# Kernel tuning notes

Hardware: AMD Instinct MI355X
Metric: run time of the kernel (lower is better)

The kernel has to match this reference:

```python
import jax, jax.numpy as jnp
import numpy as np

L = 3          # num_layers
H = 128        # hidden_dim
NH = 4         # num heads
DH = H // NH   # head dim
B = 32         # graphs per batch
N = 1024       # nodes per graph
NTOT = B * N
DEG = 16
E = NTOT * DEG
BN_EPS = 1e-5


def setup_inputs() -> dict:
    key = jax.random.key(0)
    ks = jax.random.split(key, 16)
    s = 1.0 / np.sqrt(H)
    inp = {
        "x": jax.random.normal(ks[0], (NTOT, H), jnp.float32),
        "edge_attr": jax.random.normal(ks[1], (E, H), jnp.float32),
        "gine_w1": jax.random.normal(ks[2], (L, H, H), jnp.float32) * s,
        "gine_b1": jnp.zeros((L, H), jnp.float32),
        "gine_bn_g": jnp.ones((L, H), jnp.float32),
        "gine_bn_b": jnp.zeros((L, H), jnp.float32),
        "gine_w2": jax.random.normal(ks[3], (L, H, H), jnp.float32) * s,
        "gine_b2": jnp.zeros((L, H), jnp.float32),
        "attn_wqkv": jax.random.normal(ks[4], (L, 3 * H, H), jnp.float32) * s,
        "attn_bqkv": jnp.zeros((L, 3 * H), jnp.float32),
        "attn_wo": jax.random.normal(ks[5], (L, H, H), jnp.float32) * s,
        "attn_bo": jnp.zeros((L, H), jnp.float32),
        "norm1_g": jnp.ones((L, H), jnp.float32),
        "norm1_b": jnp.zeros((L, H), jnp.float32),
        "norm2_g": jnp.ones((L, H), jnp.float32),
        "norm2_b": jnp.zeros((L, H), jnp.float32),
        "norm3_g": jnp.ones((L, H), jnp.float32),
        "norm3_b": jnp.zeros((L, H), jnp.float32),
        "mlp_w1": jax.random.normal(ks[6], (L, 2 * H, H), jnp.float32) * s,
        "mlp_b1": jnp.zeros((L, 2 * H), jnp.float32),
        "mlp_w2": jax.random.normal(ks[7], (L, H, 2 * H), jnp.float32) * (1.0 / np.sqrt(2 * H)),
        "mlp_b2": jnp.zeros((L, H), jnp.float32),
    }
    # intra-graph random edges: local src/dst in [0, N) plus per-graph offset
    offs = (jnp.arange(E, dtype=jnp.int32) // (N * DEG)) * N  # graph offset per edge
    src = jax.random.randint(ks[8], (E,), 0, N, jnp.int32) + offs
    dst = jax.random.randint(ks[9], (E,), 0, N, jnp.int32) + offs
    inp["edge_index"] = jnp.stack([src, dst]).astype(jnp.int32)
    inp["batch"] = (jnp.arange(NTOT, dtype=jnp.int32) // N)
    return inp


def _bn(x, g, b):
    m = x.mean(axis=0)
    v = jnp.var(x, axis=0)
    return (x - m) * jax.lax.rsqrt(v + BN_EPS) * g + b


def _gps_forward(x, edge_attr, gine_w1, gine_b1, gine_bn_g, gine_bn_b, gine_w2, gine_b2,
                 attn_wqkv, attn_bqkv, attn_wo, attn_bo,
                 norm1_g, norm1_b, norm2_g, norm2_b, norm3_g, norm3_b,
                 mlp_w1, mlp_b1, mlp_w2, mlp_b2, edge_index, batch):
    src, dst = edge_index[0], edge_index[1]
    for i in range(L):
        # ---- GINEConv: msg = relu(x_j + e), sum-scatter, nn-MLP on x + aggr (eps=0)
        msg = jax.nn.relu(x[src] + edge_attr)                       # [E, H]
        aggr = jax.ops.segment_sum(msg, dst, num_segments=NTOT)     # [NTOT, H]
        h = x + aggr
        h = h @ gine_w1[i].T + gine_b1[i]
        h = jax.nn.relu(_bn(h, gine_bn_g[i], gine_bn_b[i]))
        h = h @ gine_w2[i].T + gine_b2[i]
        h_local = _bn(h + x, norm1_g[i], norm1_b[i])                # residual + norm1
        # ---- global multi-head attention on x (dense per-graph, equal sizes)
        xb = x.reshape(B, N, H)
        qkv = xb @ attn_wqkv[i].T + attn_bqkv[i]                    # [B, N, 3H]
        q, k, v = jnp.split(qkv, 3, axis=-1)
        q = q.reshape(B, N, NH, DH).transpose(0, 2, 1, 3)           # [B, nh, N, dh]
        k = k.reshape(B, N, NH, DH).transpose(0, 2, 1, 3)
        v = v.reshape(B, N, NH, DH).transpose(0, 2, 1, 3)
        scores = jnp.einsum("bhqd,bhkd->bhqk", q, k) / np.sqrt(DH)
        attn = jax.nn.softmax(scores, axis=-1)
        o = jnp.einsum("bhqk,bhkd->bhqd", attn, v)
        o = o.transpose(0, 2, 1, 3).reshape(B, N, H) @ attn_wo[i].T + attn_bo[i]
        h_attn = _bn(o.reshape(NTOT, H) + x, norm2_g[i], norm2_b[i])
        # ---- combine + FFN + norm3
        out = h_local + h_attn
        ff = jax.nn.relu(out @ mlp_w1[i].T + mlp_b1[i]) @ mlp_w2[i].T + mlp_b2[i]
        x = _bn(out + ff, norm3_g[i], norm3_b[i])
        if i != L - 1:
            x = jax.nn.relu(x)
    return x


def reference(x, edge_attr, gine_w1, gine_b1, gine_bn_g, gine_bn_b, gine_w2, gine_b2,
              attn_wqkv, attn_bqkv, attn_wo, attn_bo,
              norm1_g, norm1_b, norm2_g, norm2_b, norm3_g, norm3_b,
              mlp_w1, mlp_b1, mlp_w2, mlp_b2, edge_index, batch):
    return _gps_forward(x, edge_attr, gine_w1, gine_b1, gine_bn_g, gine_bn_b, gine_w2, gine_b2,
                        attn_wqkv, attn_bqkv, attn_wo, attn_bo,
                        norm1_g, norm1_b, norm2_g, norm2_b, norm3_g, norm3_b,
                        mlp_w1, mlp_b1, mlp_w2, mlp_b2, edge_index, batch)
```

## Files before the change

kernel.cpp:

```cpp
#include <hip/hip_runtime.h>
#include <hip/hip_bf16.h>
#include <math.h>

#define NTOT 32768
#define HDIM 128
#define NE   524288
#define NGRAPH 32
#define NNODE 1024
#define NHEAD 4
#define DHEAD 32

typedef __attribute__((ext_vector_type(8))) short bf8v;
typedef __attribute__((ext_vector_type(4))) float f4v;
typedef unsigned short u16;

__device__ __forceinline__ float4 ld4(const float* p){ return *(const float4*)p; }

__device__ __forceinline__ u16 bf16rn(float f){
  union { float f; unsigned u; } x; x.f = f;
  unsigned r = x.u + 0x7FFF + ((x.u >> 16) & 1);
  return (u16)(r >> 16);
}
__device__ __forceinline__ unsigned pk2(float a, float b){
  unsigned r;
  asm("v_cvt_pk_bf16_f32 %0, %1, %2" : "=v"(r) : "v"(a), "v"(b));
  return r;
}
__device__ __forceinline__ float bf2f(u16 u){
  union { unsigned u; float f; } x; x.u = ((unsigned)u) << 16;
  return x.f;
}

__global__ void k_count(const int* __restrict__ dst, int* __restrict__ deg){
  int e = blockIdx.x*256 + threadIdx.x;
  atomicAdd(&deg[dst[e]], 1);
}

__global__ __launch_bounds__(1024) void k_scan(const int* __restrict__ deg,
                                               int* __restrict__ indptr,
                                               int* __restrict__ cursor){
  __shared__ int sm[1024];
  int t = threadIdx.x;
  int base = t*32;
  int s = 0;
  for (int j=0;j<32;j++) s += deg[base+j];
  sm[t] = s; __syncthreads();
  for (int off=1; off<1024; off<<=1){
    int v = (t>=off) ? sm[t-off] : 0;
    __syncthreads();
    sm[t] += v;
    __syncthreads();
  }
  int ex = sm[t] - s;
  for (int j=0;j<32;j++){
    int d = deg[base+j];
    indptr[base+j] = ex; cursor[base+j] = ex;
    ex += d;
  }
  if (t == 1023) indptr[NTOT] = ex;
}

__global__ void k_fill(const int* __restrict__ dst, int* __restrict__ cursor,
                       int* __restrict__ perm){
  int e = blockIdx.x*256 + threadIdx.x;
  int pos = atomicAdd(&cursor[dst[e]], 1);
  perm[pos] = e;
}

__global__ __launch_bounds__(256) void k_eaprep(const float* __restrict__ ea,
    const int* __restrict__ src, const int* __restrict__ perm,
    u16* __restrict__ EAb, int* __restrict__ SRCp){
  int tid = threadIdx.x;
  int p = blockIdx.x*8 + (tid>>5);
  int c4 = (tid&31)*4;
  int e = perm[p];
  float4 v = ld4(&ea[(size_t)e*HDIM + c4]);
  uint2 o; o.x = pk2(v.x, v.y); o.y = pk2(v.z, v.w);
  *(uint2*)&EAb[(size_t)p*HDIM + c4] = o;
  if ((tid&31) == 0) SRCp[p] = src[e];
}

__global__ __launch_bounds__(256) void k_xprep(const float* __restrict__ x, u16* __restrict__ Xb){
  size_t i = ((size_t)blockIdx.x*256 + threadIdx.x)*4;
  float4 v = ld4(&x[i]);
  uint2 o; o.x = pk2(v.x,v.y); o.y = pk2(v.z,v.w);
  *(uint2*)&Xb[i] = o;
}

__global__ __launch_bounds__(256) void k_wprep(const float* s0,const float* s1,const float* s2,
    const float* s3,const float* s4,const float* s5, u16* __restrict__ Wb){
  const float* srcs[6] = {s0,s1,s2,s3,s4,s5};
  const int cnt4[6] = {12288,12288,36864,12288,24576,24576};
  const int off[6]  = {0,49152,98304,245760,294912,393216};
  int y = blockIdx.y;
  int i = blockIdx.x*256 + threadIdx.x;
  if (i >= cnt4[y]) return;
  float4 v = ld4(&srcs[y][(size_t)i*4]);
  uint2 o; o.x = pk2(v.x,v.y); o.y = pk2(v.z,v.w);
  *(uint2*)&Wb[off[y] + (size_t)i*4] = o;
}

__global__ __launch_bounds__(256) void k_aggr(const u16* __restrict__ Xb,
                       const u16* __restrict__ EAb,
                       const int* __restrict__ SRCp, const int* __restrict__ indptr,
                       u16* __restrict__ Hb){
  int tid = threadIdx.x;
  int n = blockIdx.x*8 + (tid>>5);
  int c4 = (tid&31)*4;
  int p0 = indptr[n], p1 = indptr[n+1];
  float a0=0.f,a1=0.f,a2=0.f,a3=0.f;
  for (int p=p0;p<p1;p++){
    int s = SRCp[p];
    uint2 xv = *(const uint2*)&Xb[(size_t)s*HDIM + c4];
    uint2 ev = *(const uint2*)&EAb[(size_t)p*HDIM + c4];
    a0 += fmaxf(bf2f((u16)(xv.x&0xffff)) + bf2f((u16)(ev.x&0xffff)), 0.f);
    a1 += fmaxf(bf2f((u16)(xv.x>>16))    + bf2f((u16)(ev.x>>16)), 0.f);
    a2 += fmaxf(bf2f((u16)(xv.y&0xffff)) + bf2f((u16)(ev.y&0xffff)), 0.f);
    a3 += fmaxf(bf2f((u16)(xv.y>>16))    + bf2f((u16)(ev.y>>16)), 0.f);
  }
  uint2 xn = *(const uint2*)&Xb[(size_t)n*HDIM + c4];
  a0 += bf2f((u16)(xn.x&0xffff)); a1 += bf2f((u16)(xn.x>>16));
  a2 += bf2f((u16)(xn.y&0xffff)); a3 += bf2f((u16)(xn.y>>16));
  uint2 o; o.x = pk2(a0,a1); o.y = pk2(a2,a3);
  *(uint2*)&Hb[(size_t)n*HDIM + c4] = o;
}

template<bool BNA, bool DUAL, bool RELU, bool EP, bool STATS, bool WROUT>
__global__ __launch_bounds__(256) void k_bgemm(const u16* __restrict__ Ab,
    const u16* __restrict__ A2b,
    const float* __restrict__ slotA, const float* __restrict__ gA, const float* __restrict__ bA,
    const float* __restrict__ slotB, const float* __restrict__ gB, const float* __restrict__ bB,
    const u16* __restrict__ Wb, const float* __restrict__ bias,
    const u16* __restrict__ Epb, u16* __restrict__ Cb,
    u16* __restrict__ OUTb, float* __restrict__ slotOut, int N, int K){
  __shared__ float sbnA[256];
  __shared__ float sbnB[256];
  __shared__ float sred[128];
  int tid = threadIdx.x;
  int w = tid>>6, l = tid&63;
  int q = l&15, g = l>>4;
  int m0 = blockIdx.x*128, n0 = blockIdx.y*64;
  int wr = w*32;
  const float invn = 1.0f/32768.0f;
  if (BNA || DUAL){
    if (tid < 128){
      float mean = slotA[tid]*invn;
      float var  = slotA[128+tid]*invn - mean*mean;
      float sc = gA[tid] * rsqrtf(var + 1e-5f);
      sbnA[tid] = sc; sbnA[128+tid] = bA[tid] - mean*sc;
      if (DUAL){
        float mean2 = slotB[tid]*invn;
        float var2  = slotB[128+tid]*invn - mean2*mean2;
        float sc2 = gB[tid] * rsqrtf(var2 + 1e-5f);
        sbnB[tid] = sc2; sbnB[128+tid] = bB[tid] - mean2*sc2;
      }
    }
  }
  if (STATS && tid < 128) sred[tid] = 0.f;
  if (BNA || DUAL || STATS) __syncthreads();

  f4v acc[2][4];
  #pragma unroll
  for (int i=0;i<2;i++)
    #pragma unroll
    for (int j=0;j<4;j++) acc[i][j] = (f4v){0.f,0.f,0.f,0.f};

  for (int kc=0; kc<K; kc+=32){
    bf8v af[2], bfv[4];
    #pragma unroll
    for (int mt=0;mt<2;mt++){
      int row = m0 + wr + 16*mt + q;
      if (!BNA && !DUAL){
        af[mt] = *(const bf8v*)&Ab[(size_t)row*K + kc + 8*g];
      } else {
        union { bf8v b; u16 s[8]; unsigned u[4]; } ra, r2, ro;
        ra.b = *(const bf8v*)&Ab[(size_t)row*K + kc + 8*g];
        if (DUAL) r2.b = *(const bf8v*)&A2b[(size_t)row*K + kc + 8*g];
        float v[8];
        #pragma unroll
        for (int j=0;j<8;j++){
          int kk = kc + 8*g + j;
          float f = bf2f(ra.s[j]) * sbnA[kk] + sbnA[128+kk];
          if (BNA) f = fmaxf(f, 0.f);
          if (DUAL) f += bf2f(r2.s[j]) * sbnB[kk] + sbnB[128+kk];
          v[j] = f;
        }
        ro.u[0]=pk2(v[0],v[1]); ro.u[1]=pk2(v[2],v[3]);
        ro.u[2]=pk2(v[4],v[5]); ro.u[3]=pk2(v[6],v[7]);
        af[mt] = ro.b;
        if (WROUT && blockIdx.y == 0)
          *(uint4*)&OUTb[(size_t)row*K + kc + 8*g] = *(uint4*)ro.u;
      }
    }
    #pragma unroll
    for (int nt=0;nt<4;nt++){
      int col = n0 + 16*nt + q;
      bfv[nt] = *(const bf8v*)&Wb[(size_t)col*K + kc + 8*g];
    }
    #pragma unroll
    for (int mt=0;mt<2;mt++)
      #pragma unroll
      for (int nt=0;nt<4;nt++)
        acc[mt][nt] = __builtin_amdgcn_mfma_f32_16x16x32_bf16(af[mt], bfv[nt], acc[mt][nt], 0,0,0);
  }
  float bbv[4];
  #pragma unroll
  for (int nt=0;nt<4;nt++) bbv[nt] = bias[n0 + 16*nt + q];
  float csum[4] = {0.f,0.f,0.f,0.f}, csq[4] = {0.f,0.f,0.f,0.f};
  #pragma unroll
  for (int mt=0;mt<2;mt++){
    int row0 = m0 + wr + 16*mt + 4*g;
    #pragma unroll
    for (int nt=0;nt<4;nt++){
      int col = n0 + 16*nt + q;
      #pragma unroll
      for (int r=0;r<4;r++){
        size_t off = (size_t)(row0+r)*N + col;
        float v = acc[mt][nt][r] + bbv[nt];
        if (EP) v += bf2f(Epb[off]);
        if (RELU) v = fmaxf(v, 0.f);
        Cb[off] = bf16rn(v);
        if (STATS){ csum[nt] += v; csq[nt] += v*v; }
      }
    }
  }
  if (STATS){
    #pragma unroll
    for (int nt=0;nt<4;nt++){
      int c = 16*nt + q;
      atomicAdd(&sred[c], csum[nt]);
      atomicAdd(&sred[64+c], csq[nt]);
    }
    __syncthreads();
    if (tid < 64){
      atomicAdd(&slotOut[n0+tid], sred[tid]);
      atomicAdd(&slotOut[128+n0+tid], sred[64+tid]);
    }
  }
}

__global__ __launch_bounds__(256) void k_qkvgemm(const u16* __restrict__ Ab,
    const u16* __restrict__ Wb, const float* __restrict__ bias,
    u16* __restrict__ Qb, u16* __restrict__ Kb, u16* __restrict__ VT){
  __shared__ u16 Sm[128*72];
  int tid = threadIdx.x;
  int w = tid>>6, l = tid&63;
  int q = l&15, g = l>>4;
  int m0 = blockIdx.x*128, n0 = blockIdx.y*64;
  int which = blockIdx.y >> 1, half = blockIdx.y & 1;
  int wr = w*32;
  const int K = 128;
  f4v acc[2][4];
  #pragma unroll
  for (int i=0;i<2;i++)
    #pragma unroll
    for (int j=0;j<4;j++) acc[i][j] = (f4v){0.f,0.f,0.f,0.f};
  for (int kc=0; kc<K; kc+=32){
    bf8v af[2], bfv[4];
    #pragma unroll
    for (int mt=0;mt<2;mt++)
      af[mt] = *(const bf8v*)&Ab[(size_t)(m0+wr+16*mt+q)*K + kc + 8*g];
    #pragma unroll
    for (int nt=0;nt<4;nt++)
      bfv[nt] = *(const bf8v*)&Wb[(size_t)(n0+16*nt+q)*K + kc + 8*g];
    #pragma unroll
    for (int mt=0;mt<2;mt++)
      #pragma unroll
      for (int nt=0;nt<4;nt++)
        acc[mt][nt] = __builtin_amdgcn_mfma_f32_16x16x32_bf16(af[mt], bfv[nt], acc[mt][nt], 0,0,0);
  }
  const float QSC = 0.17677669529663687f * 1.4426950408889634f;
  float scale = (which==0) ? QSC : 1.0f;
  float bbv[4];
  #pragma unroll
  for (int nt=0;nt<4;nt++) bbv[nt] = bias[n0 + 16*nt + q];
  if (which < 2){
    #pragma unroll
    for (int mt=0;mt<2;mt++){
      int row0 = wr + 16*mt + 4*g;
      #pragma unroll
      for (int nt=0;nt<4;nt++){
        int c = 16*nt + q;
        #pragma unroll
        for (int r=0;r<4;r++)
          Sm[(row0+r)*72 + c] = bf16rn((acc[mt][nt][r] + bbv[nt]) * scale);
      }
    }
    __syncthreads();
    u16* dst = (which==0) ? Qb : Kb;
    #pragma unroll
    for (int it=0; it<4; it++){
      int idx = tid + it*256;
      int row = idx >> 3, c8 = (idx & 7) * 8;
      uint4 v = *(const uint4*)&Sm[row*72 + c8];
      *(uint4*)&dst[(size_t)(m0+row)*128 + half*64 + c8] = v;
    }
  } else {
    #pragma unroll
    for (int mt=0;mt<2;mt++){
      int row0 = wr + 16*mt + 4*g;
      #pragma unroll
      for (int nt=0;nt<4;nt++){
        int c = 16*nt + q;
        uint2 p;
        p.x = pk2(acc[mt][nt][0] + bbv[nt], acc[mt][nt][1] + bbv[nt]);
        p.y = pk2(acc[mt][nt][2] + bbv[nt], acc[mt][nt][3] + bbv[nt]);
        *(uint2*)&Sm[c*136 + row0] = p;
      }
    }
    __syncthreads();
    int gg = m0 >> 10;
    int nl0 = m0 - gg*1024;
    #pragma unroll
    for (int it=0; it<4; it++){
      int idx = tid + it*256;
      int c = idx >> 4, n8 = (idx & 15) * 8;
      uint4 v = *(const uint4*)&Sm[c*136 + n8];
      *(uint4*)&VT[((size_t)gg*128 + half*64 + c)*1024 + nl0 + n8] = v;
    }
  }
}

template<bool RELU, bool F32OUT>
__global__ __launch_bounds__(256) void k_bnapply(const u16* __restrict__ X,
    const float* __restrict__ slot, const float* __restrict__ gv, const float* __restrict__ bv,
    u16* __restrict__ Yb, float* __restrict__ Yf){
  int idx = blockIdx.x*256 + threadIdx.x;
  int row = idx >> 4, c8 = (idx & 15) * 8;
  const float invn = 1.0f/32768.0f;
  union { uint4 u; u16 s[8]; } iv;
  iv.u = *(const uint4*)&X[(size_t)row*HDIM + c8];
  float o[8];
  #pragma unroll
  for (int j=0;j<8;j++){
    int c = c8+j;
    float mean = slot[c]*invn;
    float var  = slot[128+c]*invn - mean*mean;
    float sc = gv[c] * rsqrtf(var + 1e-5f);
    float sh = bv[c] - mean*sc;
    float v = bf2f(iv.s[j])*sc + sh;
    if (RELU) v = fmaxf(v, 0.f);
    o[j] = v;
  }
  if (F32OUT){
    float* dst = &Yf[(size_t)row*HDIM + c8];
    *(float4*)dst = make_float4(o[0],o[1],o[2],o[3]);
    *(float4*)(dst+4) = make_float4(o[4],o[5],o[6],o[7]);
  } else {
    uint4 ov;
    ov.x = pk2(o[0],o[1]); ov.y = pk2(o[2],o[3]);
    ov.z = pk2(o[4],o[5]); ov.w = pk2(o[6],o[7]);
    *(uint4*)&Yb[(size_t)row*HDIM + c8] = ov;
  }
}

__global__ __launch_bounds__(256) void k_flash2(const u16* __restrict__ Qb,
    const u16* __restrict__ Kb, const u16* __restrict__ VT,
    u16* __restrict__ O){
  __shared__ u16 Pl[4][16*72];
  int tid = threadIdx.x;
  int w = tid >> 6, l = tid & 63;
  int q = l & 15, grp = l >> 4;
  int qt = blockIdx.x, h = blockIdx.y, g = blockIdx.z;
  size_t gbase = (size_t)g*1024;
  size_t qrow0 = gbase + qt*64 + w*16;
  const u16* Vp = VT + ((size_t)(g*4 + h)*32)*1024;
  bf8v qf = *(const bf8v*)&Qb[(qrow0 + q)*128 + h*32 + 8*grp];
  u16* Pw = &Pl[w][0];
  float m = -1e30f, lsum = 0.f;
  f4v o0 = {0.f,0.f,0.f,0.f}, o1 = {0.f,0.f,0.f,0.f};
  for (int kt=0; kt<16; kt++){
    int k0 = kt*64;
    f4v st[4];
    #pragma unroll
    for (int t=0;t<4;t++){
      bf8v kf = *(const bf8v*)&Kb[(gbase + k0 + 16*t + q)*128 + h*32 + 8*grp];
      st[t] = __builtin_amdgcn_mfma_f32_16x16x32_bf16(kf, qf, (f4v){0.f,0.f,0.f,0.f}, 0,0,0);
    }
    float smax = st[0][0];
    #pragma unroll
    for (int t=0;t<4;t++)
      #pragma unroll
      for (int r=0;r<4;r++) smax = fmaxf(smax, st[t][r]);
    smax = fmaxf(smax, __shfl_xor(smax, 16));
    smax = fmaxf(smax, __shfl_xor(smax, 32));
    float mnew = fmaxf(m, smax);
    float alpha = exp2f(m - mnew);
    float psum = 0.f;
    #pragma unroll
    for (int t=0;t<4;t++){
      float p0 = exp2f(st[t][0]-mnew), p1 = exp2f(st[t][1]-mnew);
      float p2 = exp2f(st[t][2]-mnew), p3 = exp2f(st[t][3]-mnew);
      psum += (p0+p1)+(p2+p3);
      *(unsigned*)&Pw[q*72 + 16*t + 4*grp]     = pk2(p0,p1);
      *(unsigned*)&Pw[q*72 + 16*t + 4*grp + 2] = pk2(p2,p3);
    }
    psum += __shfl_xor(psum, 16);
    psum += __shfl_xor(psum, 32);
    lsum = lsum*alpha + psum;
    m = mnew;
    f4v aD;
    #pragma unroll
    for (int r=0;r<4;r++) aD[r] = __shfl(alpha, 4*grp + r);
    #pragma unroll
    for (int r=0;r<4;r++){ o0[r] *= aD[r]; o1[r] *= aD[r]; }
    bf8v pa0 = *(const bf8v*)&Pw[q*72 + 8*grp];
    bf8v pa1 = *(const bf8v*)&Pw[q*72 + 32 + 8*grp];
    bf8v v00 = *(const bf8v*)&Vp[(size_t)q*1024      + k0 + 8*grp];
    bf8v v01 = *(const bf8v*)&Vp[(size_t)q*1024      + k0 + 32 + 8*grp];
    bf8v v10 = *(const bf8v*)&Vp[(size_t)(16+q)*1024 + k0 + 8*grp];
    bf8v v11 = *(const bf8v*)&Vp[(size_t)(16+q)*1024 + k0 + 32 + 8*grp];
    o0 = __builtin_amdgcn_mfma_f32_16x16x32_bf16(pa0, v00, o0, 0,0,0);
    o0 = __builtin_amdgcn_mfma_f32_16x16x32_bf16(pa1, v01, o0, 0,0,0);
    o1 = __builtin_amdgcn_mfma_f32_16x16x32_bf16(pa0, v10, o1, 0,0,0);
    o1 = __builtin_amdgcn_mfma_f32_16x16x32_bf16(pa1, v11, o1, 0,0,0);
  }
  f4v lD;
  #pragma unroll
  for (int r=0;r<4;r++) lD[r] = __shfl(lsum, 4*grp + r);
  #pragma unroll
  for (int r=0;r<4;r++){
    float inv = 1.0f/lD[r];
    size_t row = qrow0 + 4*grp + r;
    O[row*HDIM + h*32 + q]      = bf16rn(o0[r]*inv);
    O[row*HDIM + h*32 + 16 + q] = bf16rn(o1[r]*inv);
  }
}

extern "C" void kernel_launch(void* const* d_in, const int* in_sizes, int n_in,
                              void* d_out, int out_size, void* d_ws, size_t ws_size,
                              hipStream_t stream){
  const float* x_in      = (const float*)d_in[0];
  const float* edge_attr = (const float*)d_in[1];
  const float* gine_w1   = (const float*)d_in[2];
  const float* gine_b1   = (const float*)d_in[3];
  const float* gine_bn_g = (const float*)d_in[4];
  const float* gine_bn_b = (const float*)d_in[5];
  const float* gine_w2   = (const float*)d_in[6];
  const float* gine_b2   = (const float*)d_in[7];
  const float* attn_wqkv = (const float*)d_in[8];
  const float* attn_bqkv = (const float*)d_in[9];
  const float* attn_wo   = (const float*)d_in[10];
  const float* attn_bo   = (const float*)d_in[11];
  const float* norm1_g   = (const float*)d_in[12];
  const float* norm1_b   = (const float*)d_in[13];
  const float* norm2_g   = (const float*)d_in[14];
  const float* norm2_b   = (const float*)d_in[15];
  const float* norm3_g   = (const float*)d_in[16];
  const float* norm3_b   = (const float*)d_in[17];
  const float* mlp_w1    = (const float*)d_in[18];
  const float* mlp_b1    = (const float*)d_in[19];
  const float* mlp_w2    = (const float*)d_in[20];
  const float* mlp_b2    = (const float*)d_in[21];
  const int* edge_index  = (const int*)d_in[22];
  const int* srcp = edge_index;
  const int* dstp = edge_index + NE;
  float* out = (float*)d_out;

  float* ws = (float*)d_ws;
  const size_t U = 4194304;
  u16* Xb   = (u16*)(ws);
  u16* Hb   = (u16*)(ws + U/2);
  u16* G1   = (u16*)(ws + U);
  u16* P1   = (u16*)(ws + U + U/2);
  u16* P2   = (u16*)(ws + 2*U);
  u16* Ob   = (u16*)(ws + 2*U + U/2);
  u16* FFb  = (u16*)(ws + 3*U);
  u16* OUTb = (u16*)(ws + 4*U);
  u16* H3   = (u16*)(ws + 4*U + U/2);
  u16* Qb   = (u16*)(ws + 5*U);
  u16* Kb   = (u16*)(ws + 5*U + U/2);
  u16* VTb  = (u16*)(ws + 6*U);
  u16* Wball= (u16*)(ws + 6*U + U/2);
  float* STATS = ws + 7*U - 8192;
  int* IW      = (int*)(ws + 7*U);
  int* deg     = IW;
  int* indptr  = IW + 32768;
  int* cursor  = IW + 32768 + 32772;
  int* perm    = cursor + 32768;
  u16* EAb  = (u16*)(ws + 8*U);
  int* SRCp = (int*)(ws + 16*U);

  u16* W1b  = Wball + 0;
  u16* W2b  = Wball + 49152;
  u16* WQb  = Wball + 98304;
  u16* WOb  = Wball + 245760;
  u16* WM1b = Wball + 294912;
  u16* WM2b = Wball + 393216;

  hipMemsetAsync(STATS, 0, 12*512*sizeof(float), stream);
  hipMemsetAsync(deg, 0, NTOT*sizeof(int), stream);
  k_count<<<NE/256, 256, 0, stream>>>(dstp, deg);
  k_scan<<<1, 1024, 0, stream>>>(deg, indptr, cursor);
  k_fill<<<NE/256, 256, 0, stream>>>(dstp, cursor, perm);
  k_eaprep<<<NE/8, 256, 0, stream>>>(edge_attr, srcp, perm, EAb, SRCp);
  k_xprep<<<4096, 256, 0, stream>>>(x_in, Xb);
  k_wprep<<<dim3(144,6), 256, 0, stream>>>(gine_w1, gine_w2, attn_wqkv, attn_wo, mlp_w1, mlp_w2, Wball);

  dim3 gN128(NTOT/128, 2), gN256(NTOT/128, 4), gQKV(NTOT/128, 6);

  for (int i=0;i<3;i++){
    const float* B1 = gine_b1 + (size_t)i*HDIM;
    const float* B2 = gine_b2 + (size_t)i*HDIM;
    const float* BQ = attn_bqkv + (size_t)i*3*HDIM;
    const float* BO = attn_bo + (size_t)i*HDIM;
    const float* BM1 = mlp_b1 + (size_t)i*2*HDIM;
    const float* BM2 = mlp_b2 + (size_t)i*HDIM;
    u16* w1 = W1b + (size_t)i*16384;
    u16* w2 = W2b + (size_t)i*16384;
    u16* wq = WQb + (size_t)i*49152;
    u16* wo = WOb + (size_t)i*16384;
    u16* wm1 = WM1b + (size_t)i*32768;
    u16* wm2 = WM2b + (size_t)i*32768;
    float* S0 = STATS + (size_t)(i*4+0)*512;
    float* S1 = STATS + (size_t)(i*4+1)*512;
    float* S2 = STATS + (size_t)(i*4+2)*512;
    float* S3 = STATS + (size_t)(i*4+3)*512;
    const float* bnG = gine_bn_g + (size_t)i*HDIM;
    const float* bnB = gine_bn_b + (size_t)i*HDIM;
    const float* n1g = norm1_g + (size_t)i*HDIM, *n1b = norm1_b + (size_t)i*HDIM;
    const float* n2g = norm2_g + (size_t)i*HDIM, *n2b = norm2_b + (size_t)i*HDIM;
    const float* n3g = norm3_g + (size_t)i*HDIM, *n3b = norm3_b + (size_t)i*HDIM;

    k_aggr<<<NTOT/8, 256, 0, stream>>>(Xb, EAb, SRCp, indptr, Hb);
    k_bgemm<false,false,false,false,true,false><<<gN128, 256, 0, stream>>>(
      Hb, nullptr, nullptr,nullptr,nullptr, nullptr,nullptr,nullptr,
      w1, B1, nullptr, G1, nullptr, S0, 128, 128);
    k_bgemm<true,false,false,true,true,false><<<gN128, 256, 0, stream>>>(
      G1, nullptr, S0, bnG, bnB, nullptr,nullptr,nullptr,
      w2, B2, Xb, P1, nullptr, S1, 128, 128);

    k_qkvgemm<<<gQKV, 256, 0, stream>>>(Xb, wq, BQ, Qb, Kb, VTb);
    k_flash2<<<dim3(16, NHEAD, NGRAPH), 256, 0, stream>>>(Qb, Kb, VTb, Ob);
    k_bgemm<false,false,false,true,true,false><<<gN128, 256, 0, stream>>>(
      Ob, nullptr, nullptr,nullptr,nullptr, nullptr,nullptr,nullptr,
      wo, BO, Xb, P2, nullptr, S2, 128, 128);

    k_bgemm<false,true,true,false,false,true><<<gN256, 256, 0, stream>>>(
      P1, P2, S1, n1g, n1b, S2, n2g, n2b,
      wm1, BM1, nullptr, FFb, OUTb, nullptr, 256, 128);
    k_bgemm<false,false,false,true,true,false><<<gN128, 256, 0, stream>>>(
      FFb, nullptr, nullptr,nullptr,nullptr, nullptr,nullptr,nullptr,
      wm2, BM2, OUTb, H3, nullptr, S3, 128, 256);

    if (i<2) k_bnapply<true ,false><<<2048, 256, 0, stream>>>(H3, S3, n3g, n3b, Xb, nullptr);
    else     k_bnapply<false,true ><<<2048, 256, 0, stream>>>(H3, S3, n3g, n3b, nullptr, out);
  }
}
```

Baseline: 1.049 ms.

## Merge independent per-layer kernels into horizontally fused launches and combine prep kernels

Independent stages are combined into single launches that dispatch on block index: aggregation with the QKV GEMM, flash attention with the first GINE GEMM, and the two post-projection GEMMs together. The three prep kernels become one launch, with the edge-attribute scatter writing to sorted positions via an epos array in place of a perm gather. The two memsets are merged into one, and the aggregation loop prefetches the next source index. The aim is fewer launches, less tail idle time and more concurrent work per launch. The cost is shared-memory footprint set by the largest branch and possible register pressure that lowers occupancy.

```diff
diff --git a/kernel.cpp b/kernel.cpp
--- a/kernel.cpp
+++ b/kernel.cpp
@@ -61,58 +61,62 @@
 }
 
 __global__ void k_fill(const int* __restrict__ dst, int* __restrict__ cursor,
-                       int* __restrict__ perm){
+                       int* __restrict__ epos){
   int e = blockIdx.x*256 + threadIdx.x;
   int pos = atomicAdd(&cursor[dst[e]], 1);
-  perm[pos] = e;
-}
-
-__global__ __launch_bounds__(256) void k_eaprep(const float* __restrict__ ea,
-    const int* __restrict__ src, const int* __restrict__ perm,
-    u16* __restrict__ EAb, int* __restrict__ SRCp){
-  int tid = threadIdx.x;
-  int p = blockIdx.x*8 + (tid>>5);
-  int c4 = (tid&31)*4;
-  int e = perm[p];
-  float4 v = ld4(&ea[(size_t)e*HDIM + c4]);
-  uint2 o; o.x = pk2(v.x, v.y); o.y = pk2(v.z, v.w);
-  *(uint2*)&EAb[(size_t)p*HDIM + c4] = o;
-  if ((tid&31) == 0) SRCp[p] = src[e];
-}
-
-__global__ __launch_bounds__(256) void k_xprep(const float* __restrict__ x, u16* __restrict__ Xb){
-  size_t i = ((size_t)blockIdx.x*256 + threadIdx.x)*4;
-  float4 v = ld4(&x[i]);
-  uint2 o; o.x = pk2(v.x,v.y); o.y = pk2(v.z,v.w);
-  *(uint2*)&Xb[i] = o;
-}
-
-__global__ __launch_bounds__(256) void k_wprep(const float* s0,const float* s1,const float* s2,
+  epos[e] = pos;
+}
+
+__global__ __launch_bounds__(256) void k_prep(const float* __restrict__ ea,
+    const int* __restrict__ src, const int* __restrict__ epos,
+    u16* __restrict__ EAb, int* __restrict__ SRCp,
+    const float* __restrict__ x, u16* __restrict__ Xb,
+    const float* s0,const float* s1,const float* s2,
     const float* s3,const float* s4,const float* s5, u16* __restrict__ Wb){
-  const float* srcs[6] = {s0,s1,s2,s3,s4,s5};
-  const int cnt4[6] = {12288,12288,36864,12288,24576,24576};
-  const int off[6]  = {0,49152,98304,245760,294912,393216};
-  int y = blockIdx.y;
-  int i = blockIdx.x*256 + threadIdx.x;
-  if (i >= cnt4[y]) return;
-  float4 v = ld4(&srcs[y][(size_t)i*4]);
-  uint2 o; o.x = pk2(v.x,v.y); o.y = pk2(v.z,v.w);
-  *(uint2*)&Wb[off[y] + (size_t)i*4] = o;
-}
-
-__global__ __launch_bounds__(256) void k_aggr(const u16* __restrict__ Xb,
-                       const u16* __restrict__ EAb,
-                       const int* __restrict__ SRCp, const int* __restrict__ indptr,
-                       u16* __restrict__ Hb){
-  int tid = threadIdx.x;
-  int n = blockIdx.x*8 + (tid>>5);
+  int b = blockIdx.x, tid = threadIdx.x;
+  if (b < 65536){
+    int e = b*8 + (tid>>5);
+    int c4 = (tid&31)*4;
+    int pos = epos[e];
+    float4 v = ld4(&ea[(size_t)e*HDIM + c4]);
+    uint2 o; o.x = pk2(v.x, v.y); o.y = pk2(v.z, v.w);
+    *(uint2*)&EAb[(size_t)pos*HDIM + c4] = o;
+    if ((tid&31) == 0) SRCp[pos] = src[e];
+  } else if (b < 69632){
+    size_t i = ((size_t)(b-65536)*256 + tid)*4;
+    float4 v = ld4(&x[i]);
+    uint2 o; o.x = pk2(v.x,v.y); o.y = pk2(v.z,v.w);
+    *(uint2*)&Xb[i] = o;
+  } else {
+    int idx = b - 69632;
+    int y = idx / 144;
+    int i = (idx % 144)*256 + tid;
+    const float* srcs[6] = {s0,s1,s2,s3,s4,s5};
+    const int cnt4[6] = {12288,12288,36864,12288,24576,24576};
+    const int off[6]  = {0,49152,98304,245760,294912,393216};
+    if (i < cnt4[y]){
+      float4 v = ld4(&srcs[y][(size_t)i*4]);
+      uint2 o; o.x = pk2(v.x,v.y); o.y = pk2(v.z,v.w);
+      *(uint2*)&Wb[off[y] + (size_t)i*4] = o;
+    }
+  }
+}
+
+__device__ __forceinline__ void aggr_body(int bx, int tid,
+    const u16* __restrict__ Xb, const u16* __restrict__ EAb,
+    const int* __restrict__ SRCp, const int* __restrict__ indptr,
+    u16* __restrict__ Hb){
+  int n = bx*8 + (tid>>5);
   int c4 = (tid&31)*4;
   int p0 = indptr[n], p1 = indptr[n+1];
   float a0=0.f,a1=0.f,a2=0.f,a3=0.f;
-  for (int p=p0;p<p1;p++){
-    int s = SRCp[p];
+  int p = p0;
+  int sNext = (p < p1) ? SRCp[p] : 0;
+  for (; p<p1; p++){
+    int s = sNext;
+    if (p+1 < p1) sNext = SRCp[p+1];
+    uint2 ev = *(const uint2*)&EAb[(size_t)p*HDIM + c4];
     uint2 xv = *(const uint2*)&Xb[(size_t)s*HDIM + c4];
-    uint2 ev = *(const uint2*)&EAb[(size_t)p*HDIM + c4];
     a0 += fmaxf(bf2f((u16)(xv.x&0xffff)) + bf2f((u16)(ev.x&0xffff)), 0.f);
     a1 += fmaxf(bf2f((u16)(xv.x>>16))    + bf2f((u16)(ev.x>>16)), 0.f);
     a2 += fmaxf(bf2f((u16)(xv.y&0xffff)) + bf2f((u16)(ev.y&0xffff)), 0.f);
@@ -126,34 +130,29 @@
 }
 
 template<bool BNA, bool DUAL, bool RELU, bool EP, bool STATS, bool WROUT>
-__global__ __launch_bounds__(256) void k_bgemm(const u16* __restrict__ Ab,
-    const u16* __restrict__ A2b,
+__device__ __forceinline__ void bgemm_body(int bx, int by, int tid,
+    const u16* __restrict__ Ab, const u16* __restrict__ A2b,
     const float* __restrict__ slotA, const float* __restrict__ gA, const float* __restrict__ bA,
     const float* __restrict__ slotB, const float* __restrict__ gB, const float* __restrict__ bB,
     const u16* __restrict__ Wb, const float* __restrict__ bias,
     const u16* __restrict__ Epb, u16* __restrict__ Cb,
-    u16* __restrict__ OUTb, float* __restrict__ slotOut, int N, int K){
-  __shared__ float sbnA[256];
-  __shared__ float sbnB[256];
-  __shared__ float sred[128];
-  int tid = threadIdx.x;
+    u16* __restrict__ OUTb, float* __restrict__ slotOut, int N, int K,
+    float* sbn1, float* sbn2, float* sred){
   int w = tid>>6, l = tid&63;
   int q = l&15, g = l>>4;
-  int m0 = blockIdx.x*128, n0 = blockIdx.y*64;
+  int m0 = bx*128, n0 = by*64;
   int wr = w*32;
   const float invn = 1.0f/32768.0f;
-  if (BNA || DUAL){
-    if (tid < 128){
-      float mean = slotA[tid]*invn;
-      float var  = slotA[128+tid]*invn - mean*mean;
-      float sc = gA[tid] * rsqrtf(var + 1e-5f);
-      sbnA[tid] = sc; sbnA[128+tid] = bA[tid] - mean*sc;
-      if (DUAL){
-        float mean2 = slotB[tid]*invn;
-        float var2  = slotB[128+tid]*invn - mean2*mean2;
-        float sc2 = gB[tid] * rsqrtf(var2 + 1e-5f);
-        sbnB[tid] = sc2; sbnB[128+tid] = bB[tid] - mean2*sc2;
-      }
+  if ((BNA || DUAL) && tid < 128){
+    float mean = slotA[tid]*invn;
+    float var  = slotA[128+tid]*invn - mean*mean;
+    float s = gA[tid] * rsqrtf(var + 1e-5f);
+    sbn1[tid] = s; sbn1[128+tid] = bA[tid] - mean*s;
+    if (DUAL){
+      float mean2 = slotB[tid]*invn;
+      float var2  = slotB[128+tid]*invn - mean2*mean2;
+      float s2 = gB[tid] * rsqrtf(var2 + 1e-5f);
+      sbn2[tid] = s2; sbn2[128+tid] = bB[tid] - mean2*s2;
     }
   }
   if (STATS && tid < 128) sred[tid] = 0.f;
@@ -166,7 +165,7 @@
     for (int j=0;j<4;j++) acc[i][j] = (f4v){0.f,0.f,0.f,0.f};
 
   for (int kc=0; kc<K; kc+=32){
-    bf8v af[2], bfv[4];
+    bf8v af[2];
     #pragma unroll
     for (int mt=0;mt<2;mt++){
       int row = m0 + wr + 16*mt + q;
@@ -180,23 +179,22 @@
         #pragma unroll
         for (int j=0;j<8;j++){
           int kk = kc + 8*g + j;
-          float f = bf2f(ra.s[j]) * sbnA[kk] + sbnA[128+kk];
+          float f = bf2f(ra.s[j]) * sbn1[kk] + sbn1[128+kk];
           if (BNA) f = fmaxf(f, 0.f);
-          if (DUAL) f += bf2f(r2.s[j]) * sbnB[kk] + sbnB[128+kk];
+          if (DUAL) f += bf2f(r2.s[j]) * sbn2[kk] + sbn2[128+kk];
           v[j] = f;
         }
         ro.u[0]=pk2(v[0],v[1]); ro.u[1]=pk2(v[2],v[3]);
         ro.u[2]=pk2(v[4],v[5]); ro.u[3]=pk2(v[6],v[7]);
         af[mt] = ro.b;
-        if (WROUT && blockIdx.y == 0)
+        if (WROUT && by == 0)
           *(uint4*)&OUTb[(size_t)row*K + kc + 8*g] = *(uint4*)ro.u;
       }
     }
-    #pragma unroll
-    for (int nt=0;nt<4;nt++){
-      int col = n0 + 16*nt + q;
-      bfv[nt] = *(const bf8v*)&Wb[(size_t)col*K + kc + 8*g];
-    }
+    bf8v bfv[4];
+    #pragma unroll
+    for (int nt=0;nt<4;nt++)
+      bfv[nt] = *(const bf8v*)&Wb[(size_t)(n0+16*nt+q)*K + kc + 8*g];
     #pragma unroll
     for (int mt=0;mt<2;mt++)
       #pragma unroll
@@ -239,27 +237,26 @@
   }
 }
 
-__global__ __launch_bounds__(256) void k_qkvgemm(const u16* __restrict__ Ab,
-    const u16* __restrict__ Wb, const float* __restrict__ bias,
-    u16* __restrict__ Qb, u16* __restrict__ Kb, u16* __restrict__ VT){
-  __shared__ u16 Sm[128*72];
-  int tid = threadIdx.x;
+__device__ __forceinline__ void qkv_body(int bx, int by, int tid,
+    const u16* __restrict__ Ab, const u16* __restrict__ Wb, const float* __restrict__ bias,
+    u16* __restrict__ Qb, u16* __restrict__ Kb, u16* __restrict__ VT, u16* Sm){
   int w = tid>>6, l = tid&63;
   int q = l&15, g = l>>4;
-  int m0 = blockIdx.x*128, n0 = blockIdx.y*64;
-  int which = blockIdx.y >> 1, half = blockIdx.y & 1;
+  int which = by >> 1, half = by & 1;
+  int m0 = bx*128, n0 = by*64;
+  const int K = 128;
   int wr = w*32;
-  const int K = 128;
   f4v acc[2][4];
   #pragma unroll
   for (int i=0;i<2;i++)
     #pragma unroll
     for (int j=0;j<4;j++) acc[i][j] = (f4v){0.f,0.f,0.f,0.f};
   for (int kc=0; kc<K; kc+=32){
-    bf8v af[2], bfv[4];
+    bf8v af[2];
     #pragma unroll
     for (int mt=0;mt<2;mt++)
       af[mt] = *(const bf8v*)&Ab[(size_t)(m0+wr+16*mt+q)*K + kc + 8*g];
+    bf8v bfv[4];
     #pragma unroll
     for (int nt=0;nt<4;nt++)
       bfv[nt] = *(const bf8v*)&Wb[(size_t)(n0+16*nt+q)*K + kc + 8*g];
@@ -310,7 +307,7 @@
     }
     __syncthreads();
     int gg = m0 >> 10;
-    int nl0 = m0 - gg*1024;
+    int nl0 = m0 & 1023;
     #pragma unroll
     for (int it=0; it<4; it++){
       int idx = tid + it*256;
@@ -321,52 +318,16 @@
   }
 }
 
-template<bool RELU, bool F32OUT>
-__global__ __launch_bounds__(256) void k_bnapply(const u16* __restrict__ X,
-    const float* __restrict__ slot, const float* __restrict__ gv, const float* __restrict__ bv,
-    u16* __restrict__ Yb, float* __restrict__ Yf){
-  int idx = blockIdx.x*256 + threadIdx.x;
-  int row = idx >> 4, c8 = (idx & 15) * 8;
-  const float invn = 1.0f/32768.0f;
-  union { uint4 u; u16 s[8]; } iv;
-  iv.u = *(const uint4*)&X[(size_t)row*HDIM + c8];
-  float o[8];
-  #pragma unroll
-  for (int j=0;j<8;j++){
-    int c = c8+j;
-    float mean = slot[c]*invn;
-    float var  = slot[128+c]*invn - mean*mean;
-    float sc = gv[c] * rsqrtf(var + 1e-5f);
-    float sh = bv[c] - mean*sc;
-    float v = bf2f(iv.s[j])*sc + sh;
-    if (RELU) v = fmaxf(v, 0.f);
-    o[j] = v;
-  }
-  if (F32OUT){
-    float* dst = &Yf[(size_t)row*HDIM + c8];
-    *(float4*)dst = make_float4(o[0],o[1],o[2],o[3]);
-    *(float4*)(dst+4) = make_float4(o[4],o[5],o[6],o[7]);
-  } else {
-    uint4 ov;
-    ov.x = pk2(o[0],o[1]); ov.y = pk2(o[2],o[3]);
-    ov.z = pk2(o[4],o[5]); ov.w = pk2(o[6],o[7]);
-    *(uint4*)&Yb[(size_t)row*HDIM + c8] = ov;
-  }
-}
-
-__global__ __launch_bounds__(256) void k_flash2(const u16* __restrict__ Qb,
-    const u16* __restrict__ Kb, const u16* __restrict__ VT,
-    u16* __restrict__ O){
-  __shared__ u16 Pl[4][16*72];
-  int tid = threadIdx.x;
+__device__ __forceinline__ void flash_body(int qt, int h, int g, int tid,
+    const u16* __restrict__ Qb, const u16* __restrict__ Kb, const u16* __restrict__ VT,
+    u16* __restrict__ O, u16* Pl){
   int w = tid >> 6, l = tid & 63;
   int q = l & 15, grp = l >> 4;
-  int qt = blockIdx.x, h = blockIdx.y, g = blockIdx.z;
   size_t gbase = (size_t)g*1024;
   size_t qrow0 = gbase + qt*64 + w*16;
   const u16* Vp = VT + ((size_t)(g*4 + h)*32)*1024;
   bf8v qf = *(const bf8v*)&Qb[(qrow0 + q)*128 + h*32 + 8*grp];
-  u16* Pw = &Pl[w][0];
+  u16* Pw = Pl + w*(16*72);
   float m = -1e30f, lsum = 0.f;
   f4v o0 = {0.f,0.f,0.f,0.f}, o1 = {0.f,0.f,0.f,0.f};
   for (int kt=0; kt<16; kt++){
@@ -424,6 +385,111 @@
     size_t row = qrow0 + 4*grp + r;
     O[row*HDIM + h*32 + q]      = bf16rn(o0[r]*inv);
     O[row*HDIM + h*32 + 16 + q] = bf16rn(o1[r]*inv);
+  }
+}
+
+__global__ __launch_bounds__(256) void k_d1(const u16* __restrict__ Xb,
+    const u16* __restrict__ EAb, const int* __restrict__ SRCp, const int* __restrict__ indptr,
+    u16* __restrict__ Hb,
+    const u16* __restrict__ wq, const float* __restrict__ BQ,
+    u16* __restrict__ Qb, u16* __restrict__ Kb, u16* __restrict__ VTb){
+  __shared__ u16 Sm[128*72];
+  int bx = blockIdx.x;
+  if (bx < 4096){
+    aggr_body(bx, threadIdx.x, Xb, EAb, SRCp, indptr, Hb);
+  } else {
+    int b = bx - 4096;
+    qkv_body(b & 255, b >> 8, threadIdx.x, Xb, wq, BQ, Qb, Kb, VTb, Sm);
+  }
+}
+
+__global__ __launch_bounds__(256) void k_d2(const u16* __restrict__ Qb,
+    const u16* __restrict__ Kb, const u16* __restrict__ VTb, u16* __restrict__ Ob,
+    const u16* __restrict__ Hb, const u16* __restrict__ w1, const float* __restrict__ B1,
+    u16* __restrict__ G1, float* __restrict__ S0){
+  __shared__ u16 Pl[4*16*72];
+  __shared__ float sb1[256], sb2[256], sr[128];
+  int bx = blockIdx.x;
+  if (bx < 2048){
+    flash_body(bx & 15, (bx >> 4) & 3, bx >> 6, threadIdx.x, Qb, Kb, VTb, Ob, Pl);
+  } else {
+    int b = bx - 2048;
+    bgemm_body<false,false,false,false,true,false>(b & 255, b >> 8, threadIdx.x,
+      Hb, nullptr, nullptr,nullptr,nullptr, nullptr,nullptr,nullptr,
+      w1, B1, nullptr, G1, nullptr, S0, 128, 128, sb1, sb2, sr);
+  }
+}
+
+__global__ __launch_bounds__(256) void k_d3(const u16* __restrict__ G1,
+    const float* __restrict__ S0, const float* __restrict__ bnG, const float* __restrict__ bnB,
+    const u16* __restrict__ w2, const float* __restrict__ B2,
+    const u16* __restrict__ Xb, u16* __restrict__ P1, float* __restrict__ S1,
+    const u16* __restrict__ Ob, const u16* __restrict__ wo, const float* __restrict__ BO,
+    u16* __restrict__ P2, float* __restrict__ S2){
+  __shared__ float sb1[256], sb2[256], sr[128];
+  int bx = blockIdx.x;
+  if (bx < 512){
+    bgemm_body<true,false,false,true,true,false>(bx & 255, bx >> 8, threadIdx.x,
+      G1, nullptr, S0, bnG, bnB, nullptr,nullptr,nullptr,
+      w2, B2, Xb, P1, nullptr, S1, 128, 128, sb1, sb2, sr);
+  } else {
+    int b = bx - 512;
+    bgemm_body<false,false,false,true,true,false>(b & 255, b >> 8, threadIdx.x,
+      Ob, nullptr, nullptr,nullptr,nullptr, nullptr,nullptr,nullptr,
+      wo, BO, Xb, P2, nullptr, S2, 128, 128, sb1, sb2, sr);
+  }
+}
+
+__global__ __launch_bounds__(256) void k_mlp1(const u16* __restrict__ P1, const u16* __restrict__ P2,
+    const float* __restrict__ S1, const float* __restrict__ n1g, const float* __restrict__ n1b,
+    const float* __restrict__ S2, const float* __restrict__ n2g, const float* __restrict__ n2b,
+    const u16* __restrict__ wm1, const float* __restrict__ BM1,
+    u16* __restrict__ FFb, u16* __restrict__ OUTb){
+  __shared__ float sb1[256], sb2[256], sr[128];
+  bgemm_body<false,true,true,false,false,true>(blockIdx.x, blockIdx.y, threadIdx.x,
+    P1, P2, S1, n1g, n1b, S2, n2g, n2b,
+    wm1, BM1, nullptr, FFb, OUTb, nullptr, 256, 128, sb1, sb2, sr);
+}
+
+__global__ __launch_bounds__(256) void k_mlp2(const u16* __restrict__ FFb,
+    const u16* __restrict__ wm2, const float* __restrict__ BM2,
+    const u16* __restrict__ OUTb, u16* __restrict__ H3, float* __restrict__ S3){
+  __shared__ float sb1[256], sb2[256], sr[128];
+  bgemm_body<false,false,false,true,true,false>(blockIdx.x, blockIdx.y, threadIdx.x,
+    FFb, nullptr, nullptr,nullptr,nullptr, nullptr,nullptr,nullptr,
+    wm2, BM2, OUTb, H3, nullptr, S3, 128, 256, sb1, sb2, sr);
+}
+
+template<bool RELU, bool F32OUT>
+__global__ __launch_bounds__(256) void k_bnapply(const u16* __restrict__ X,
+    const float* __restrict__ slot, const float* __restrict__ gv, const float* __restrict__ bv,
+    u16* __restrict__ Yb, float* __restrict__ Yf){
+  int idx = blockIdx.x*256 + threadIdx.x;
+  int row = idx >> 4, c8 = (idx & 15) * 8;
+  const float invn = 1.0f/32768.0f;
+  union { uint4 u; u16 s[8]; } iv;
+  iv.u = *(const uint4*)&X[(size_t)row*HDIM + c8];
+  float o[8];
+  #pragma unroll
+  for (int j=0;j<8;j++){
+    int c = c8+j;
+    float mean = slot[c]*invn;
+    float var  = slot[128+c]*invn - mean*mean;
+    float sc = gv[c] * rsqrtf(var + 1e-5f);
+    float sh = bv[c] - mean*sc;
+    float v = bf2f(iv.s[j])*sc + sh;
+    if (RELU) v = fmaxf(v, 0.f);
+    o[j] = v;
+  }
+  if (F32OUT){
+    float* dst = &Yf[(size_t)row*HDIM + c8];
+    *(float4*)dst = make_float4(o[0],o[1],o[2],o[3]);
+    *(float4*)(dst+4) = make_float4(o[4],o[5],o[6],o[7]);
+  } else {
+    uint4 ov;
+    ov.x = pk2(o[0],o[1]); ov.y = pk2(o[2],o[3]);
+    ov.z = pk2(o[4],o[5]); ov.w = pk2(o[6],o[7]);
+    *(uint4*)&Yb[(size_t)row*HDIM + c8] = ov;
   }
 }
 
@@ -477,7 +543,7 @@
   int* deg     = IW;
   int* indptr  = IW + 32768;
   int* cursor  = IW + 32768 + 32772;
-  int* perm    = cursor + 32768;
+  int* epos    = cursor + 32768;
   u16* EAb  = (u16*)(ws + 8*U);
   int* SRCp = (int*)(ws + 16*U);
 
@@ -488,16 +554,12 @@
   u16* WM1b = Wball + 294912;
   u16* WM2b = Wball + 393216;
 
-  hipMemsetAsync(STATS, 0, 12*512*sizeof(float), stream);
-  hipMemsetAsync(deg, 0, NTOT*sizeof(int), stream);
+  hipMemsetAsync(STATS, 0, 8192*sizeof(float) + NTOT*sizeof(int), stream);
   k_count<<<NE/256, 256, 0, stream>>>(dstp, deg);
   k_scan<<<1, 1024, 0, stream>>>(deg, indptr, cursor);
-  k_fill<<<NE/256, 256, 0, stream>>>(dstp, cursor, perm);
-  k_eaprep<<<NE/8, 256, 0, stream>>>(edge_attr, srcp, perm, EAb, SRCp);
-  k_xprep<<<4096, 256, 0, stream>>>(x_in, Xb);
-  k_wprep<<<dim3(144,6), 256, 0, stream>>>(gine_w1, gine_w2, attn_wqkv, attn_wo, mlp_w1, mlp_w2, Wball);
-
-  dim3 gN128(NTOT/128, 2), gN256(NTOT/128, 4), gQKV(NTOT/128, 6);
+  k_fill<<<NE/256, 256, 0, stream>>>(dstp, cursor, epos);
+  k_prep<<<70496, 256, 0, stream>>>(edge_attr, srcp, epos, EAb, SRCp, x_in, Xb,
+                                    gine_w1, gine_w2, attn_wqkv, attn_wo, mlp_w1, mlp_w2, Wball);
 
   for (int i=0;i<3;i++){
     const float* B1 = gine_b1 + (size_t)i*HDIM;
@@ -522,26 +584,13 @@
     const float* n2g = norm2_g + (size_t)i*HDIM, *n2b = norm2_b + (size_t)i*HDIM;
     const float* n3g = norm3_g + (size_t)i*HDIM, *n3b = norm3_b + (size_t)i*HDIM;
 
-    k_aggr<<<NTOT/8, 256, 0, stream>>>(Xb, EAb, SRCp, indptr, Hb);
-    k_bgemm<false,false,false,false,true,false><<<gN128, 256, 0, stream>>>(
-      Hb, nullptr, nullptr,nullptr,nullptr, nullptr,nullptr,nullptr,
-      w1, B1, nullptr, G1, nullptr, S0, 128, 128);
-    k_bgemm<true,false,false,true,true,false><<<gN128, 256, 0, stream>>>(
-      G1, nullptr, S0, bnG, bnB, nullptr,nullptr,nullptr,
-      w2, B2, Xb, P1, nullptr, S1, 128, 128);
-
-    k_qkvgemm<<<gQKV, 256, 0, stream>>>(Xb, wq, BQ, Qb, Kb, VTb);
-    k_flash2<<<dim3(16, NHEAD, NGRAPH), 256, 0, stream>>>(Qb, Kb, VTb, Ob);
-    k_bgemm<false,false,false,true,true,false><<<gN128, 256, 0, stream>>>(
-      Ob, nullptr, nullptr,nullptr,nullptr, nullptr,nullptr,nullptr,
-      wo, BO, Xb, P2, nullptr, S2, 128, 128);
-
-    k_bgemm<false,true,true,false,false,true><<<gN256, 256, 0, stream>>>(
-      P1, P2, S1, n1g, n1b, S2, n2g, n2b,
-      wm1, BM1, nullptr, FFb, OUTb, nullptr, 256, 128);
-    k_bgemm<false,false,false,true,true,false><<<gN128, 256, 0, stream>>>(
-      FFb, nullptr, nullptr,nullptr,nullptr, nullptr,nullptr,nullptr,
-      wm2, BM2, OUTb, H3, nullptr, S3, 128, 256);
+    k_d1<<<5632, 256, 0, stream>>>(Xb, EAb, SRCp, indptr, Hb, wq, BQ, Qb, Kb, VTb);
+    k_d2<<<2560, 256, 0, stream>>>(Qb, Kb, VTb, Ob, Hb, w1, B1, G1, S0);
+    k_d3<<<1024, 256, 0, stream>>>(G1, S0, bnG, bnB, w2, B2, Xb, P1, S1,
+                                   Ob, wo, BO, P2, S2);
+    k_mlp1<<<dim3(256,4), 256, 0, stream>>>(P1, P2, S1, n1g, n1b, S2, n2g, n2b,
+                                            wm1, BM1, FFb, OUTb);
+    k_mlp2<<<dim3(256,2), 256, 0, stream>>>(FFb, wm2, BM2, OUTb, H3, S3);
 
     if (i<2) k_bnapply<true ,false><<<2048, 256, 0, stream>>>(H3, S3, n3g, n3b, Xb, nullptr);
     else     k_bnapply<false,true ><<<2048, 256, 0, stream>>>(H3, S3, n3g, n3b, nullptr, out);
```

New measurement: 982.4 us. 6.3% less time.
